# Kernel optimization log

Measured on AMD Instinct MI355X. Metric: run time of the kernel, lower is better.

The kernel has to match this reference:

```python
import jax, jax.numpy as jnp
import numpy as np

B, TA, TB, DIN, DEMB = 32, 128, 1024, 1280, 512
LN_EPS = 1e-5
MM_EPS = 1e-6


def _param(key, shape, scale=0.02):
    return (jax.random.normal(key, shape, dtype=jnp.float32) * scale)


def setup_inputs() -> dict:
    key = jax.random.key(0)
    ks = jax.random.split(key, 24)
    inp = {
        'pep_esm': jax.random.normal(ks[0], (B, TA, DIN), dtype=jnp.float32),
        'rec_esm': jax.random.normal(ks[1], (B, TB, DIN), dtype=jnp.float32),
        'pep_mask': jax.random.randint(ks[2], (B, TA), 0, 2, dtype=jnp.int32),
        'rec_mask': jax.random.randint(ks[3], (B, TB), 0, 2, dtype=jnp.int32),
        'temperature': jnp.asarray(1.0, dtype=jnp.float32),
    }
    i = 4
    for pre in ('pep', 'rec'):
        inp[pre + '_pw'] = _param(ks[i], (DIN, DEMB)); i += 1
        inp[pre + '_pb'] = jnp.zeros((DEMB,), jnp.float32)
        inp[pre + '_f1w'] = _param(ks[i], (DEMB, DEMB)); i += 1
        inp[pre + '_f1b'] = jnp.zeros((DEMB,), jnp.float32)
        inp[pre + '_lng'] = jnp.ones((DEMB,), jnp.float32)
        inp[pre + '_lnb'] = jnp.zeros((DEMB,), jnp.float32)
        inp[pre + '_f2w'] = _param(ks[i], (DEMB, DEMB)); i += 1
        inp[pre + '_f2b'] = jnp.zeros((DEMB,), jnp.float32)
    return inp


def _encode(x, pw, pb, f1w, f1b, lng, lnb, f2w, f2b):
    # projection -> (Linear, ReLU, LayerNorm) -> final Linear (dropout=0 at eval)
    e = x @ pw + pb                                   # [b, t, DEMB]
    h = jax.nn.relu(e @ f1w + f1b)
    mu = h.mean(-1, keepdims=True)
    var = ((h - mu) ** 2).mean(-1, keepdims=True)
    h = (h - mu) * jax.lax.rsqrt(var + LN_EPS) * lng + lnb
    out = h @ f2w + f2b
    return out / jnp.linalg.norm(out, axis=-1, keepdims=True)


def _masked_mean(t, mask, axis=-1):
    numer = jnp.where(mask, t, 0.0).sum(axis=axis)
    denom = jnp.maximum(mask.sum(axis=axis).astype(t.dtype), MM_EPS)
    return numer / denom


def reference(pep_esm, rec_esm, pep_mask, rec_mask, temperature,
              pep_pw, pep_pb, pep_f1w, pep_f1b, pep_lng, pep_lnb, pep_f2w, pep_f2b,
              rec_pw, rec_pb, rec_f1w, rec_f1b, rec_lng, rec_lnb, rec_f2w, rec_f2b):
    hA = _encode(pep_esm, pep_pw, pep_pb, pep_f1w, pep_f1b, pep_lng, pep_lnb, pep_f2w, pep_f2b)
    hB = _encode(rec_esm, rec_pw, rec_pb, rec_f1w, rec_f1b, rec_lng, rec_lnb, rec_f2w, rec_f2b)
    mA = pep_mask.astype(bool)                        # [bA, tA]
    mB = rec_mask.astype(bool)                        # [bB, tB]
    # pairwise token similarity: [bA, bB, tA, tB]
    sim = jnp.einsum('atd,bsd->abts', hA, hB) / temperature
    cmask = mA[:, None, :, None] & mB[None, :, None, :]
    neg = jnp.finfo(sim.dtype).min
    sim_m = jnp.where(cmask, sim, neg)
    sA = sim_m.max(axis=-1)                            # [bA, bB, tA]
    sB = sim_m.max(axis=-2)                            # [bA, bB, tB]
    sim_scores_A = _masked_mean(sA, mA[:, None, :])    # [bA, bB]
    sim_scores_B = _masked_mean(sB, mB[None, :, :])    # [bA, bB]
    return sim_scores_A, sim_scores_B
```

## Files before the change

### kernel.cpp

```cpp
#include <hip/hip_runtime.h>
#include <float.h>
#include <stddef.h>
#include <stdint.h>

#define DIN_   1280
#define DEMB_  512
#define NBAT_  32
#define TA_    128
#define TB_    1024
#define LN_EPS_ 1e-5f

using short8  = __attribute__((ext_vector_type(8))) short;
using ushort8 = __attribute__((ext_vector_type(8))) unsigned short;
using f32x4   = __attribute__((ext_vector_type(4))) float;

typedef const __attribute__((address_space(1))) unsigned int gu32;
typedef __attribute__((address_space(3))) unsigned int lu32;

__device__ __forceinline__ void gld_lds16(const void* g, void* l) {
    __builtin_amdgcn_global_load_lds((gu32*)g, (lu32*)l, 16, 0, 0);
}

__device__ __forceinline__ unsigned short f2bf(float x) {
    unsigned u = __float_as_uint(x);
    u += 0x7FFFu + ((u >> 16) & 1u);
    return (unsigned short)(u >> 16);
}
__device__ __forceinline__ float bf2f(unsigned short u) {
    return __uint_as_float((unsigned)u << 16);
}
__device__ __forceinline__ int clampi(int v, int hi) {
    return v < 0 ? 0 : (v > hi ? hi : v);
}

__global__ __launch_bounds__(64) void compact_idx_kernel(
    const int* __restrict__ mask, int T, int* __restrict__ idx, int* __restrict__ cnt)
{
    const int b = blockIdx.x, lane = threadIdx.x;
    const int base = b * T;
    int run = 0;
    for (int c = 0; c < T; c += 64) {
        int m = mask[base + c + lane] != 0;
        unsigned long long bal = __ballot(m);
        int pos = run + __popcll(bal & ((1ull << lane) - 1ull));
        idx[base + c + lane] = m ? pos : -1;
        run += __popcll(bal);
    }
    if (lane == 0) cnt[b] = run;
}

__global__ __launch_bounds__(64) void offsets_kernel(
    const int* __restrict__ cntA, const int* __restrict__ cntB,
    int* __restrict__ offA, int* __restrict__ offB, int* __restrict__ tot)
{
    if (threadIdx.x == 0) {
        int s = 0;
        for (int i = 0; i < NBAT_; ++i) { offA[i] = s; s += cntA[i]; }
        tot[0] = s;
        s = 0;
        for (int i = 0; i < NBAT_; ++i) { offB[i] = s; s += cntB[i]; }
        tot[1] = s;
    }
}

__global__ __launch_bounds__(256) void srcrows_kernel(
    const int* __restrict__ idx, const int* __restrict__ off, int shift,
    int* __restrict__ srcrows)
{
    int r = blockIdx.x * 256 + threadIdx.x;
    int d = idx[r];
    if (d >= 0) srcrows[off[r >> shift] + d] = r;
}

struct WPack { const float* src[4]; unsigned short* dst[4]; };
__global__ __launch_bounds__(256) void wtrans_multi_kernel(WPack p, int K, int N)
{
    __shared__ float tile[32][33];
    const float* W = p.src[blockIdx.z];
    unsigned short* Wt = p.dst[blockIdx.z];
    const int k0 = blockIdx.x * 32, n0 = blockIdx.y * 32;
    const int r = threadIdx.x >> 5, c = threadIdx.x & 31;
    #pragma unroll
    for (int i = 0; i < 4; ++i)
        tile[r + i * 8][c] = W[(size_t)(k0 + r + i * 8) * N + n0 + c];
    __syncthreads();
    #pragma unroll
    for (int i = 0; i < 4; ++i)
        Wt[(size_t)(n0 + r + i * 8) * K + k0 + c] = f2bf(tile[c][r + i * 8]);
}

struct EncDual {
    const unsigned short* A[2];
    const unsigned short* Wt[2];
    const float* bias[2];
    unsigned short* C[2];
    const int* Nr[2];
};
struct ProjDual {
    const float* A[2];
    const unsigned short* Wt[2];
    const float* bias[2];
    unsigned short* C[2];
    const int* srcrows[2];
    const int* Nr[2];
    int Mmax[2];
};
struct LnDual { unsigned short* h[2]; const float* g[2]; const float* b[2]; const int* Nr[2]; };
struct L2Dual { const unsigned short* h[2]; unsigned short* o[2]; const int* Nr[2]; };

template<int K, bool RELU>
__global__ __launch_bounds__(512, 4) void egemm_bf16_dual(EncDual P)
{
    const int side = blockIdx.y;
    const int bid = blockIdx.x;
    const int row0 = (bid >> 2) * 128, col0 = (bid & 3) * 128;
    if (row0 >= *P.Nr[side]) return;
    const unsigned short* A = P.A[side];
    const unsigned short* Wt = P.Wt[side];
    const float* bias = P.bias[side];
    unsigned short* C = P.C[side];

    __shared__ __align__(16) unsigned char Abuf[128 * 64 * 2];
    __shared__ __align__(16) unsigned char Bbuf[128 * 64 * 2];
    const int t = threadIdx.x;
    const int wave = t >> 6, lane = t & 63;
    const int wr = wave >> 2, wc = wave & 3;
    const int cl = lane & 15, rg = lane >> 4;

    const int pr0 = t >> 3, pq0 = t & 7;
    const int pr1 = pr0 + 64;
    const int ks0 = ((pq0 ^ (pr0 & 7)) * 8);
    const int ks1 = ((pq0 ^ (pr1 & 7)) * 8);
    const unsigned short* Aglob = A + (size_t)row0 * K;
    const unsigned short* Bglob = Wt + (size_t)col0 * K;

    int aoff[4], asw[4], boff[2], bsw[2];
    #pragma unroll
    for (int m = 0; m < 4; ++m) {
        int r = wr * 64 + m * 16 + cl;
        aoff[m] = r * 128; asw[m] = (r & 7) << 4;
    }
    #pragma unroll
    for (int n = 0; n < 2; ++n) {
        int c = wc * 32 + n * 16 + cl;
        boff[n] = c * 128; bsw[n] = (c & 7) << 4;
    }

    f32x4 acc[4][2];
    #pragma unroll
    for (int m = 0; m < 4; ++m) {
        acc[m][0] = (f32x4){0.f, 0.f, 0.f, 0.f};
        acc[m][1] = (f32x4){0.f, 0.f, 0.f, 0.f};
    }
    for (int k0 = 0; k0 < K; k0 += 64) {
        gld_lds16(Aglob + (size_t)pr0 * K + k0 + ks0, Abuf + t * 16);
        gld_lds16(Aglob + (size_t)pr1 * K + k0 + ks1, Abuf + (t + 512) * 16);
        gld_lds16(Bglob + (size_t)pr0 * K + k0 + ks0, Bbuf + t * 16);
        gld_lds16(Bglob + (size_t)pr1 * K + k0 + ks1, Bbuf + (t + 512) * 16);
        __syncthreads();
        #pragma unroll
        for (int h = 0; h < 2; ++h) {
            const int cb = h * 64 + rg * 16;
            short8 av[4], bv[2];
            #pragma unroll
            for (int m = 0; m < 4; ++m)
                av[m] = *(const short8*)(Abuf + aoff[m] + (cb ^ asw[m]));
            #pragma unroll
            for (int n = 0; n < 2; ++n)
                bv[n] = *(const short8*)(Bbuf + boff[n] + (cb ^ bsw[n]));
            #pragma unroll
            for (int m = 0; m < 4; ++m)
                #pragma unroll
                for (int n = 0; n < 2; ++n)
                    acc[m][n] = __builtin_amdgcn_mfma_f32_16x16x32_bf16(
                        av[m], bv[n], acc[m][n], 0, 0, 0);
        }
        __syncthreads();
    }
    const float b0 = bias[col0 + wc * 32 + cl];
    const float b1 = bias[col0 + wc * 32 + 16 + cl];
    #pragma unroll
    for (int m = 0; m < 4; ++m)
        #pragma unroll
        for (int j = 0; j < 4; ++j) {
            int row = row0 + wr * 64 + m * 16 + rg * 4 + j;
            float v0 = acc[m][0][j] + b0;
            float v1 = acc[m][1][j] + b1;
            if (RELU) { v0 = fmaxf(v0, 0.f); v1 = fmaxf(v1, 0.f); }
            C[(size_t)row * DEMB_ + col0 + wc * 32 + cl]      = f2bf(v0);
            C[(size_t)row * DEMB_ + col0 + wc * 32 + 16 + cl] = f2bf(v1);
        }
}

template<int K, bool RELU>
__global__ __launch_bounds__(512, 4) void egemm_f32a_g_dual(ProjDual P)
{
    const int side = blockIdx.y;
    const int bid = blockIdx.x;
    const int row0 = (bid >> 2) * 128, col0 = (bid & 3) * 128;
    if (row0 >= *P.Nr[side]) return;
    const float* A = P.A[side];
    const unsigned short* Wt = P.Wt[side];
    const float* bias = P.bias[side];
    unsigned short* C = P.C[side];
    const int* srcrows = P.srcrows[side];
    const int Mmax = P.Mmax[side];

    __shared__ __align__(16) unsigned char Abuf[128 * 64 * 2];
    __shared__ __align__(16) unsigned char Bbuf[128 * 64 * 2];
    const int t = threadIdx.x;
    const int wave = t >> 6, lane = t & 63;
    const int wr = wave >> 2, wc = wave & 3;
    const int cl = lane & 15, rg = lane >> 4;

    const int pr0 = t >> 3, pq0 = t & 7;
    const int pr1 = pr0 + 64;
    const int ks0 = ((pq0 ^ (pr0 & 7)) * 8);
    const int ks1 = ((pq0 ^ (pr1 & 7)) * 8);
    const int ad0 = pr0 * 128 + ((pq0 ^ (pr0 & 7)) << 4);
    const int ad1 = pr1 * 128 + ((pq0 ^ (pr1 & 7)) << 4);
    const int sr0 = clampi(srcrows[row0 + pr0], Mmax - 1);
    const int sr1 = clampi(srcrows[row0 + pr1], Mmax - 1);
    const float* Ar0 = A + (size_t)sr0 * K;
    const float* Ar1 = A + (size_t)sr1 * K;
    const unsigned short* Bglob = Wt + (size_t)col0 * K;

    int aoff[4], asw[4], boff[2], bsw[2];
    #pragma unroll
    for (int m = 0; m < 4; ++m) {
        int r = wr * 64 + m * 16 + cl;
        aoff[m] = r * 128; asw[m] = (r & 7) << 4;
    }
    #pragma unroll
    for (int n = 0; n < 2; ++n) {
        int c = wc * 32 + n * 16 + cl;
        boff[n] = c * 128; bsw[n] = (c & 7) << 4;
    }

    f32x4 acc[4][2];
    #pragma unroll
    for (int m = 0; m < 4; ++m) {
        acc[m][0] = (f32x4){0.f, 0.f, 0.f, 0.f};
        acc[m][1] = (f32x4){0.f, 0.f, 0.f, 0.f};
    }
    for (int k0 = 0; k0 < K; k0 += 64) {
        gld_lds16(Bglob + (size_t)pr0 * K + k0 + ks0, Bbuf + t * 16);
        gld_lds16(Bglob + (size_t)pr1 * K + k0 + ks1, Bbuf + (t + 512) * 16);
        {
            const float* s0 = Ar0 + k0 + pq0 * 8;
            const float* s1 = Ar1 + k0 + pq0 * 8;
            float4 u0 = *(const float4*)(s0), u1 = *(const float4*)(s0 + 4);
            float4 u2 = *(const float4*)(s1), u3 = *(const float4*)(s1 + 4);
            ushort8 w0, w1;
            w0[0] = f2bf(u0.x); w0[1] = f2bf(u0.y); w0[2] = f2bf(u0.z); w0[3] = f2bf(u0.w);
            w0[4] = f2bf(u1.x); w0[5] = f2bf(u1.y); w0[6] = f2bf(u1.z); w0[7] = f2bf(u1.w);
            w1[0] = f2bf(u2.x); w1[1] = f2bf(u2.y); w1[2] = f2bf(u2.z); w1[3] = f2bf(u2.w);
            w1[4] = f2bf(u3.x); w1[5] = f2bf(u3.y); w1[6] = f2bf(u3.z); w1[7] = f2bf(u3.w);
            *(ushort8*)(Abuf + ad0) = w0;
            *(ushort8*)(Abuf + ad1) = w1;
        }
        __syncthreads();
        #pragma unroll
        for (int h = 0; h < 2; ++h) {
            const int cb = h * 64 + rg * 16;
            short8 av[4], bv[2];
            #pragma unroll
            for (int m = 0; m < 4; ++m)
                av[m] = *(const short8*)(Abuf + aoff[m] + (cb ^ asw[m]));
            #pragma unroll
            for (int n = 0; n < 2; ++n)
                bv[n] = *(const short8*)(Bbuf + boff[n] + (cb ^ bsw[n]));
            #pragma unroll
            for (int m = 0; m < 4; ++m)
                #pragma unroll
                for (int n = 0; n < 2; ++n)
                    acc[m][n] = __builtin_amdgcn_mfma_f32_16x16x32_bf16(
                        av[m], bv[n], acc[m][n], 0, 0, 0);
        }
        __syncthreads();
    }
    const float b0 = bias[col0 + wc * 32 + cl];
    const float b1 = bias[col0 + wc * 32 + 16 + cl];
    #pragma unroll
    for (int m = 0; m < 4; ++m)
        #pragma unroll
        for (int j = 0; j < 4; ++j) {
            int row = row0 + wr * 64 + m * 16 + rg * 4 + j;
            float v0 = acc[m][0][j] + b0;
            float v1 = acc[m][1][j] + b1;
            if (RELU) { v0 = fmaxf(v0, 0.f); v1 = fmaxf(v1, 0.f); }
            C[(size_t)row * DEMB_ + col0 + wc * 32 + cl]      = f2bf(v0);
            C[(size_t)row * DEMB_ + col0 + wc * 32 + 16 + cl] = f2bf(v1);
        }
}

__global__ __launch_bounds__(256) void ln_bf16_dual(LnDual P)
{
    const int side = blockIdx.y;
    const int lane = threadIdx.x & 63;
    const int row = blockIdx.x * 4 + (threadIdx.x >> 6);
    if (row >= *P.Nr[side]) return;
    unsigned short* p = P.h[side] + (size_t)row * DEMB_;
    const float* g = P.g[side];
    const float* b = P.b[side];
    ushort8 v = *(const ushort8*)(p + lane * 8);
    float x[8];
    #pragma unroll
    for (int i = 0; i < 8; ++i) x[i] = bf2f(v[i]);
    float s = 0.f;
    #pragma unroll
    for (int i = 0; i < 8; ++i) s += x[i];
    #pragma unroll
    for (int d = 32; d >= 1; d >>= 1) s += __shfl_xor(s, d);
    float mu = s * (1.f / DEMB_);
    float sq = 0.f;
    #pragma unroll
    for (int i = 0; i < 8; ++i) { float dd = x[i] - mu; sq += dd * dd; }
    #pragma unroll
    for (int d = 32; d >= 1; d >>= 1) sq += __shfl_xor(sq, d);
    float rs = 1.f / sqrtf(sq * (1.f / DEMB_) + LN_EPS_);
    float4 g0 = *(const float4*)(g + lane * 8);
    float4 g1 = *(const float4*)(g + lane * 8 + 4);
    float4 b0 = *(const float4*)(b + lane * 8);
    float4 b1 = *(const float4*)(b + lane * 8 + 4);
    float gg[8] = {g0.x, g0.y, g0.z, g0.w, g1.x, g1.y, g1.z, g1.w};
    float bb[8] = {b0.x, b0.y, b0.z, b0.w, b1.x, b1.y, b1.z, b1.w};
    ushort8 o;
    #pragma unroll
    for (int i = 0; i < 8; ++i) o[i] = f2bf((x[i] - mu) * rs * gg[i] + bb[i]);
    *(ushort8*)(p + lane * 8) = o;
}

__global__ __launch_bounds__(256) void l2norm_bf16_dual(L2Dual P)
{
    const int side = blockIdx.y;
    const int lane = threadIdx.x & 63;
    const int row = blockIdx.x * 4 + (threadIdx.x >> 6);
    if (row >= *P.Nr[side]) return;
    const unsigned short* p = P.h[side] + (size_t)row * DEMB_;
    ushort8 v = *(const ushort8*)(p + lane * 8);
    float x[8];
    #pragma unroll
    for (int i = 0; i < 8; ++i) x[i] = bf2f(v[i]);
    float sq = 0.f;
    #pragma unroll
    for (int i = 0; i < 8; ++i) sq += x[i] * x[i];
    #pragma unroll
    for (int d = 32; d >= 1; d >>= 1) sq += __shfl_xor(sq, d);
    float rs = 1.f / sqrtf(sq);
    ushort8 w;
    #pragma unroll
    for (int i = 0; i < 8; ++i) w[i] = f2bf(x[i] * rs);
    *(ushort8*)(P.o[side] + (size_t)row * DEMB_ + lane * 8) = w;
}

__global__ __launch_bounds__(128, 3) void sim_part_kernel(
    const unsigned short* __restrict__ hA,
    const unsigned short* __restrict__ hB,
    const int* __restrict__ offA, const int* __restrict__ cntA,
    const int* __restrict__ offB, const int* __restrict__ cntB,
    const float* __restrict__ temp,
    float* __restrict__ rowmax_ws,
    float* __restrict__ colmax_ws)
{
    __shared__ __align__(16) unsigned char Abuf[64 * 64 * 2];
    __shared__ __align__(16) unsigned char Bbuf[128 * 64 * 2];
    __shared__ float rowpart[2][64];

    const int bid = blockIdx.x;
    const int g = (bid & 7) * 2048 + (bid >> 3);
    const int b = g >> 9;
    const int a = (g >> 4) & 31;
    const int at = (g >> 3) & 1, a0 = at << 6;
    const int s0t = g & 7, s0 = s0t << 7;

    const int nBb = cntB[b];
    if (s0 >= nBb) return;
    const int nAa = cntA[a];
    if (a0 >= nAa) return;

    const int t = threadIdx.x;
    const int w = t >> 6, lane = t & 63;
    const int cl = lane & 15, rg = lane >> 4;
    const float invT = 1.0f / temp[0];

    const int pr = t >> 3, pq = t & 7;
    const int ks = (pq ^ (pr & 7)) * 8;
    const int abase = offA[a] + a0 + pr;
    const int bbase = offB[b] + s0 + pr;
    const unsigned short* Ap[4];
    const unsigned short* Bp[8];
    #pragma unroll
    for (int i = 0; i < 4; ++i)
        Ap[i] = hA + (size_t)clampi(abase + 16 * i, NBAT_ * TA_ - 1) * DEMB_ + ks;
    #pragma unroll
    for (int i = 0; i < 8; ++i)
        Bp[i] = hB + (size_t)clampi(bbase + 16 * i, NBAT_ * TB_ - 1) * DEMB_ + ks;

    unsigned mabits = 0;
    #pragma unroll
    for (int m = 0; m < 4; ++m)
        #pragma unroll
        for (int j = 0; j < 4; ++j)
            if (a0 + m * 16 + rg * 4 + j < nAa) mabits |= 1u << (m * 4 + j);
    int mb[4];
    #pragma unroll
    for (int n = 0; n < 4; ++n)
        mb[n] = (s0 + w * 64 + n * 16 + cl) < nBb;

    int aoff[4], asw[4], boff[4], bsw[4];
    #pragma unroll
    for (int m = 0; m < 4; ++m) {
        int r = m * 16 + cl;
        aoff[m] = r * 128; asw[m] = (r & 7) << 4;
    }
    #pragma unroll
    for (int n = 0; n < 4; ++n) {
        int c = w * 64 + n * 16 + cl;
        boff[n] = c * 128; bsw[n] = (c & 7) << 4;
    }

    f32x4 acc[4][4];
    #pragma unroll
    for (int m = 0; m < 4; ++m)
        #pragma unroll
        for (int n = 0; n < 4; ++n)
            acc[m][n] = (f32x4){0.f, 0.f, 0.f, 0.f};

    for (int k0 = 0; k0 < DEMB_; k0 += 64) {
        #pragma unroll
        for (int i = 0; i < 4; ++i)
            gld_lds16(Ap[i] + k0, Abuf + (t + 128 * i) * 16);
        #pragma unroll
        for (int i = 0; i < 8; ++i)
            gld_lds16(Bp[i] + k0, Bbuf + (t + 128 * i) * 16);
        __syncthreads();
        #pragma unroll
        for (int h = 0; h < 2; ++h) {
            const int cb = h * 64 + rg * 16;
            short8 av[4], bv[4];
            #pragma unroll
            for (int m = 0; m < 4; ++m)
                av[m] = *(const short8*)(Abuf + aoff[m] + (cb ^ asw[m]));
            #pragma unroll
            for (int n = 0; n < 4; ++n)
                bv[n] = *(const short8*)(Bbuf + boff[n] + (cb ^ bsw[n]));
            #pragma unroll
            for (int m = 0; m < 4; ++m)
                #pragma unroll
                for (int n = 0; n < 4; ++n)
                    acc[m][n] = __builtin_amdgcn_mfma_f32_16x16x32_bf16(
                        av[m], bv[n], acc[m][n], 0, 0, 0);
        }
        __syncthreads();
    }
    float rmax[4][4];
    float cmax[4] = {-FLT_MAX, -FLT_MAX, -FLT_MAX, -FLT_MAX};
    #pragma unroll
    for (int m = 0; m < 4; ++m)
        #pragma unroll
        for (int j = 0; j < 4; ++j) {
            const bool ra = (mabits >> (m * 4 + j)) & 1;
            float rm = -FLT_MAX;
            #pragma unroll
            for (int n = 0; n < 4; ++n) {
                float v = (ra && mb[n]) ? acc[m][n][j] * invT : -FLT_MAX;
                rm = fmaxf(rm, v);
                cmax[n] = fmaxf(cmax[n], v);
            }
            rmax[m][j] = rm;
        }
    #pragma unroll
    for (int d = 1; d < 16; d <<= 1)
        #pragma unroll
        for (int m = 0; m < 4; ++m)
            #pragma unroll
            for (int j = 0; j < 4; ++j)
                rmax[m][j] = fmaxf(rmax[m][j], __shfl_xor(rmax[m][j], d));
    if (cl == 0) {
        #pragma unroll
        for (int m = 0; m < 4; ++m)
            #pragma unroll
            for (int j = 0; j < 4; ++j)
                rowpart[w][m * 16 + rg * 4 + j] = rmax[m][j];
    }
    #pragma unroll
    for (int n = 0; n < 4; ++n) {
        cmax[n] = fmaxf(cmax[n], __shfl_xor(cmax[n], 16));
        cmax[n] = fmaxf(cmax[n], __shfl_xor(cmax[n], 32));
    }
    if (rg == 0) {
        float* cw = colmax_ws + ((size_t)((a * NBAT_ + b) * 2 + at)) * TB_ + s0;
        #pragma unroll
        for (int n = 0; n < 4; ++n)
            cw[w * 64 + n * 16 + cl] = cmax[n];
    }
    __syncthreads();
    if (t < 64) {
        float r = fmaxf(rowpart[0][t], rowpart[1][t]);
        rowmax_ws[(((size_t)(a * NBAT_ + b)) * 8 + s0t) * 128 + a0 + t] = r;
    }
}

__global__ __launch_bounds__(256) void sim_reduce_kernel(
    const float* __restrict__ rowmax_ws, const float* __restrict__ colmax_ws,
    const int* __restrict__ cntA, const int* __restrict__ cntB,
    float* __restrict__ out)
{
    __shared__ float red[4][2];
    const int bid = blockIdx.x;
    const int a = bid >> 5, b = bid & 31;
    const int t = threadIdx.x, lane = t & 63, wave = t >> 6;
    const int nAa = cntA[a], nBb = cntB[b];
    const int nt = (nBb + 127) >> 7;

    float numA = 0.f, sumB = 0.f;
    if (t < 128 && t < nAa) {
        const float* rp = rowmax_ws + ((size_t)(a * NBAT_ + b)) * 8 * 128 + t;
        float r = -FLT_MAX;
        for (int s = 0; s < nt; ++s) r = fmaxf(r, rp[s * 128]);
        numA = r;
    }
    const float* cp0 = colmax_ws + ((size_t)(a * NBAT_ + b)) * 2 * TB_;
    const float* cp1 = cp0 + TB_;
    const bool two = nAa > 64;
    #pragma unroll
    for (int i = 0; i < 4; ++i) {
        int s = t + i * 256;
        if (s < nBb) {
            float v = cp0[s];
            if (two) v = fmaxf(v, cp1[s]);
            sumB += v;
        }
    }
    #pragma unroll
    for (int d = 32; d >= 1; d >>= 1) {
        numA += __shfl_xor(numA, d);
        sumB += __shfl_xor(sumB, d);
    }
    if (lane == 0) { red[wave][0] = numA; red[wave][1] = sumB; }
    __syncthreads();
    if (t == 0) {
        float n  = red[0][0] + red[1][0] + red[2][0] + red[3][0];
        float nb = red[0][1] + red[1][1] + red[2][1] + red[3][1];
        out[a * NBAT_ + b] = n / fmaxf((float)nAa, 1e-6f);
        out[NBAT_ * NBAT_ + a * NBAT_ + b] = nb / fmaxf((float)nBb, 1e-6f);
    }
}

extern "C" void kernel_launch(void* const* d_in, const int* in_sizes, int n_in,
                              void* d_out, int out_size, void* d_ws, size_t ws_size,
                              hipStream_t stream)
{
    const float* pep_esm  = (const float*)d_in[0];
    const float* rec_esm  = (const float*)d_in[1];
    const int*   pep_mask = (const int*)d_in[2];
    const int*   rec_mask = (const int*)d_in[3];
    const float* temp     = (const float*)d_in[4];
    const float* pep_pw  = (const float*)d_in[5];
    const float* pep_pb  = (const float*)d_in[6];
    const float* pep_f1w = (const float*)d_in[7];
    const float* pep_f1b = (const float*)d_in[8];
    const float* pep_lng = (const float*)d_in[9];
    const float* pep_lnb = (const float*)d_in[10];
    const float* pep_f2w = (const float*)d_in[11];
    const float* pep_f2b = (const float*)d_in[12];
    const float* rec_pw  = (const float*)d_in[13];
    const float* rec_pb  = (const float*)d_in[14];
    const float* rec_f1w = (const float*)d_in[15];
    const float* rec_f1b = (const float*)d_in[16];
    const float* rec_lng = (const float*)d_in[17];
    const float* rec_lnb = (const float*)d_in[18];
    const float* rec_f2w = (const float*)d_in[19];
    const float* rec_f2b = (const float*)d_in[20];
    float* out = (float*)d_out;

    const int Mr = NBAT_ * TB_;
    const int Mp = NBAT_ * TA_;

    char* base = (char*)d_ws;
    unsigned short* R1    = (unsigned short*)(base);
    unsigned short* R2    = (unsigned short*)(base + ((size_t)32 << 20));
    unsigned short* hB_c  = (unsigned short*)(base + ((size_t)64 << 20));
    unsigned short* hA_c  = (unsigned short*)(base + ((size_t)96 << 20));
    unsigned short* wts   = (unsigned short*)(base + ((size_t)101 << 20));
    unsigned short* rec_pwt  = wts;
    unsigned short* pep_pwt  = rec_pwt + 512 * 1280;
    unsigned short* rec_f1wt = pep_pwt + 512 * 1280;
    unsigned short* rec_f2wt = rec_f1wt + 512 * 512;
    unsigned short* pep_f1wt = rec_f2wt + 512 * 512;
    unsigned short* pep_f2wt = pep_f1wt + 512 * 512;
    unsigned short* P1 = (unsigned short*)(base + ((size_t)106 << 20));
    unsigned short* P2 = (unsigned short*)(base + ((size_t)110 << 20));
    float* rowmax_ws = (float*)(base + ((size_t)106 << 20));
    float* colmax_ws = (float*)(base + ((size_t)110 << 20));
    int* idxA = (int*)(base + ((size_t)118 << 20));
    int* idxB = idxA + Mp;
    int* cntA = idxB + Mr;
    int* cntB = cntA + NBAT_;
    int* offA = cntB + NBAT_;
    int* offB = offA + NBAT_;
    int* tot  = offB + NBAT_;
    int* srcA = tot + 2;
    int* srcB = srcA + Mp;

    dim3 b256(256);
    compact_idx_kernel<<<dim3(NBAT_), dim3(64), 0, stream>>>(pep_mask, TA_, idxA, cntA);
    compact_idx_kernel<<<dim3(NBAT_), dim3(64), 0, stream>>>(rec_mask, TB_, idxB, cntB);
    offsets_kernel<<<dim3(1), dim3(64), 0, stream>>>(cntA, cntB, offA, offB, tot);
    srcrows_kernel<<<dim3(Mp / 256), b256, 0, stream>>>(idxA, offA, 7, srcA);
    srcrows_kernel<<<dim3(Mr / 256), b256, 0, stream>>>(idxB, offB, 10, srcB);

    {
        WPack p1; p1.src[0] = rec_pw; p1.dst[0] = rec_pwt;
                  p1.src[1] = pep_pw; p1.dst[1] = pep_pwt;
                  p1.src[2] = rec_pw; p1.dst[2] = rec_pwt;
                  p1.src[3] = rec_pw; p1.dst[3] = rec_pwt;
        wtrans_multi_kernel<<<dim3(DIN_ / 32, DEMB_ / 32, 2), b256, 0, stream>>>(p1, DIN_, DEMB_);
        WPack p2; p2.src[0] = rec_f1w; p2.dst[0] = rec_f1wt;
                  p2.src[1] = rec_f2w; p2.dst[1] = rec_f2wt;
                  p2.src[2] = pep_f1w; p2.dst[2] = pep_f1wt;
                  p2.src[3] = pep_f2w; p2.dst[3] = pep_f2wt;
        wtrans_multi_kernel<<<dim3(DEMB_ / 32, DEMB_ / 32, 4), b256, 0, stream>>>(p2, DEMB_, DEMB_);
    }

    const int* NrRec = tot + 1;
    const int* NrPep = tot;
    const dim3 ggrid((Mr / 128) * 4, 2);
    const dim3 ngrid(Mr / 4, 2);

    {
        ProjDual P;
        P.A[0] = rec_esm;  P.A[1] = pep_esm;
        P.Wt[0] = rec_pwt; P.Wt[1] = pep_pwt;
        P.bias[0] = rec_pb; P.bias[1] = pep_pb;
        P.C[0] = R1; P.C[1] = P1;
        P.srcrows[0] = srcB; P.srcrows[1] = srcA;
        P.Nr[0] = NrRec; P.Nr[1] = NrPep;
        P.Mmax[0] = Mr; P.Mmax[1] = Mp;
        egemm_f32a_g_dual<DIN_, false><<<ggrid, dim3(512), 0, stream>>>(P);
    }
    {
        EncDual P;
        P.A[0] = R1; P.A[1] = P1;
        P.Wt[0] = rec_f1wt; P.Wt[1] = pep_f1wt;
        P.bias[0] = rec_f1b; P.bias[1] = pep_f1b;
        P.C[0] = R2; P.C[1] = P2;
        P.Nr[0] = NrRec; P.Nr[1] = NrPep;
        egemm_bf16_dual<DEMB_, true><<<ggrid, dim3(512), 0, stream>>>(P);
    }
    {
        LnDual P;
        P.h[0] = R2; P.h[1] = P2;
        P.g[0] = rec_lng; P.g[1] = pep_lng;
        P.b[0] = rec_lnb; P.b[1] = pep_lnb;
        P.Nr[0] = NrRec; P.Nr[1] = NrPep;
        ln_bf16_dual<<<ngrid, b256, 0, stream>>>(P);
    }
    {
        EncDual P;
        P.A[0] = R2; P.A[1] = P2;
        P.Wt[0] = rec_f2wt; P.Wt[1] = pep_f2wt;
        P.bias[0] = rec_f2b; P.bias[1] = pep_f2b;
        P.C[0] = R1; P.C[1] = P1;
        P.Nr[0] = NrRec; P.Nr[1] = NrPep;
        egemm_bf16_dual<DEMB_, false><<<ggrid, dim3(512), 0, stream>>>(P);
    }
    {
        L2Dual P;
        P.h[0] = R1; P.h[1] = P1;
        P.o[0] = hB_c; P.o[1] = hA_c;
        P.Nr[0] = NrRec; P.Nr[1] = NrPep;
        l2norm_bf16_dual<<<ngrid, b256, 0, stream>>>(P);
    }

    sim_part_kernel<<<dim3(NBAT_ * NBAT_ * 2 * 8), dim3(128), 0, stream>>>(
        hA_c, hB_c, offA, cntA, offB, cntB, temp, rowmax_ws, colmax_ws);
    sim_reduce_kernel<<<dim3(NBAT_ * NBAT_), b256, 0, stream>>>(
        rowmax_ws, colmax_ws, cntA, cntB, out);
}
```

Measured before the change: 264.4 us.

## Double-buffer LDS tiles in similarity GEMM to overlap loads with MFMA

New measurement: 302.0 us. 1.14x slower.

```diff
diff --git a/kernel.cpp b/kernel.cpp
--- a/kernel.cpp
+++ b/kernel.cpp
@@ -363,8 +363,8 @@
     float* __restrict__ rowmax_ws,
     float* __restrict__ colmax_ws)
 {
-    __shared__ __align__(16) unsigned char Abuf[64 * 64 * 2];
-    __shared__ __align__(16) unsigned char Bbuf[128 * 64 * 2];
+    __shared__ __align__(16) unsigned char Abuf[2 * 64 * 64 * 2];
+    __shared__ __align__(16) unsigned char Bbuf[2 * 128 * 64 * 2];
     __shared__ float rowpart[2][64];
 
     const int bid = blockIdx.x;
@@ -427,24 +427,42 @@
         for (int n = 0; n < 4; ++n)
             acc[m][n] = (f32x4){0.f, 0.f, 0.f, 0.f};
 
-    for (int k0 = 0; k0 < DEMB_; k0 += 64) {
-        #pragma unroll
-        for (int i = 0; i < 4; ++i)
-            gld_lds16(Ap[i] + k0, Abuf + (t + 128 * i) * 16);
-        #pragma unroll
-        for (int i = 0; i < 8; ++i)
-            gld_lds16(Bp[i] + k0, Bbuf + (t + 128 * i) * 16);
-        __syncthreads();
+    #pragma unroll
+    for (int i = 0; i < 4; ++i)
+        gld_lds16(Ap[i], Abuf + (t + 128 * i) * 16);
+    #pragma unroll
+    for (int i = 0; i < 8; ++i)
+        gld_lds16(Bp[i], Bbuf + (t + 128 * i) * 16);
+
+    int cur = 0;
+    for (int k = 0; k < 8; ++k) {
+        if (k < 7) {
+            const int k1 = (k + 1) * 64;
+            const int poA = (cur ^ 1) * 8192;
+            const int poB = (cur ^ 1) * 16384;
+            #pragma unroll
+            for (int i = 0; i < 4; ++i)
+                gld_lds16(Ap[i] + k1, Abuf + poA + (t + 128 * i) * 16);
+            #pragma unroll
+            for (int i = 0; i < 8; ++i)
+                gld_lds16(Bp[i] + k1, Bbuf + poB + (t + 128 * i) * 16);
+            asm volatile("s_waitcnt vmcnt(12)" ::: "memory");
+        } else {
+            asm volatile("s_waitcnt vmcnt(0)" ::: "memory");
+        }
+        __builtin_amdgcn_s_barrier();
+        const int boA = cur * 8192;
+        const int boB = cur * 16384;
         #pragma unroll
         for (int h = 0; h < 2; ++h) {
             const int cb = h * 64 + rg * 16;
             short8 av[4], bv[4];
             #pragma unroll
             for (int m = 0; m < 4; ++m)
-                av[m] = *(const short8*)(Abuf + aoff[m] + (cb ^ asw[m]));
+                av[m] = *(const short8*)(Abuf + boA + aoff[m] + (cb ^ asw[m]));
             #pragma unroll
             for (int n = 0; n < 4; ++n)
-                bv[n] = *(const short8*)(Bbuf + boff[n] + (cb ^ bsw[n]));
+                bv[n] = *(const short8*)(Bbuf + boB + boff[n] + (cb ^ bsw[n]));
             #pragma unroll
             for (int m = 0; m < 4; ++m)
                 #pragma unroll
@@ -452,7 +470,9 @@
                     acc[m][n] = __builtin_amdgcn_mfma_f32_16x16x32_bf16(
                         av[m], bv[n], acc[m][n], 0, 0, 0);
         }
-        __syncthreads();
+        asm volatile("s_waitcnt lgkmcnt(0)" ::: "memory");
+        __builtin_amdgcn_s_barrier();
+        cur ^= 1;
     }
     float rmax[4][4];
     float cmax[4] = {-FLT_MAX, -FLT_MAX, -FLT_MAX, -FLT_MAX};
```

## Use a single wave per 64x128 sim tile with 4x8 MFMA accumulators

Applied to the files above, without the earlier changes.

Measured after the change: 272.4 us. 3.0% more time.

```diff
diff --git a/kernel.cpp b/kernel.cpp
--- a/kernel.cpp
+++ b/kernel.cpp
@@ -354,7 +354,7 @@
     *(ushort8*)(P.o[side] + (size_t)row * DEMB_ + lane * 8) = w;
 }
 
-__global__ __launch_bounds__(128, 3) void sim_part_kernel(
+__global__ __launch_bounds__(64, 2) void sim_part_kernel(
     const unsigned short* __restrict__ hA,
     const unsigned short* __restrict__ hB,
     const int* __restrict__ offA, const int* __restrict__ cntA,
@@ -365,7 +365,6 @@
 {
     __shared__ __align__(16) unsigned char Abuf[64 * 64 * 2];
     __shared__ __align__(16) unsigned char Bbuf[128 * 64 * 2];
-    __shared__ float rowpart[2][64];
 
     const int bid = blockIdx.x;
     const int g = (bid & 7) * 2048 + (bid >> 3);
@@ -380,22 +379,21 @@
     if (a0 >= nAa) return;
 
     const int t = threadIdx.x;
-    const int w = t >> 6, lane = t & 63;
-    const int cl = lane & 15, rg = lane >> 4;
+    const int cl = t & 15, rg = t >> 4;
     const float invT = 1.0f / temp[0];
 
-    const int pr = t >> 3, pq = t & 7;
-    const int ks = (pq ^ (pr & 7)) * 8;
-    const int abase = offA[a] + a0 + pr;
-    const int bbase = offB[b] + s0 + pr;
-    const unsigned short* Ap[4];
-    const unsigned short* Bp[8];
-    #pragma unroll
-    for (int i = 0; i < 4; ++i)
-        Ap[i] = hA + (size_t)clampi(abase + 16 * i, NBAT_ * TA_ - 1) * DEMB_ + ks;
+    const int tr = t >> 3, tq = t & 7;
+    const int ks = (tq ^ tr) * 8;
+    const int abase = offA[a] + a0 + tr;
+    const int bbase = offB[b] + s0 + tr;
+    const unsigned short* Ap[8];
+    const unsigned short* Bp[16];
     #pragma unroll
     for (int i = 0; i < 8; ++i)
-        Bp[i] = hB + (size_t)clampi(bbase + 16 * i, NBAT_ * TB_ - 1) * DEMB_ + ks;
+        Ap[i] = hA + (size_t)clampi(abase + 8 * i, NBAT_ * TA_ - 1) * DEMB_ + ks;
+    #pragma unroll
+    for (int i = 0; i < 16; ++i)
+        Bp[i] = hB + (size_t)clampi(bbase + 8 * i, NBAT_ * TB_ - 1) * DEMB_ + ks;
 
     unsigned mabits = 0;
     #pragma unroll
@@ -403,59 +401,61 @@
         #pragma unroll
         for (int j = 0; j < 4; ++j)
             if (a0 + m * 16 + rg * 4 + j < nAa) mabits |= 1u << (m * 4 + j);
-    int mb[4];
-    #pragma unroll
-    for (int n = 0; n < 4; ++n)
-        mb[n] = (s0 + w * 64 + n * 16 + cl) < nBb;
-
-    int aoff[4], asw[4], boff[4], bsw[4];
+    int mb[8];
+    #pragma unroll
+    for (int n = 0; n < 8; ++n)
+        mb[n] = (s0 + n * 16 + cl) < nBb;
+
+    int aoff[4], asw[4], boff[8], bsw[8];
     #pragma unroll
     for (int m = 0; m < 4; ++m) {
         int r = m * 16 + cl;
         aoff[m] = r * 128; asw[m] = (r & 7) << 4;
     }
     #pragma unroll
-    for (int n = 0; n < 4; ++n) {
-        int c = w * 64 + n * 16 + cl;
+    for (int n = 0; n < 8; ++n) {
+        int c = n * 16 + cl;
         boff[n] = c * 128; bsw[n] = (c & 7) << 4;
     }
 
-    f32x4 acc[4][4];
+    f32x4 acc[4][8];
     #pragma unroll
     for (int m = 0; m < 4; ++m)
         #pragma unroll
-        for (int n = 0; n < 4; ++n)
+        for (int n = 0; n < 8; ++n)
             acc[m][n] = (f32x4){0.f, 0.f, 0.f, 0.f};
 
     for (int k0 = 0; k0 < DEMB_; k0 += 64) {
         #pragma unroll
-        for (int i = 0; i < 4; ++i)
-            gld_lds16(Ap[i] + k0, Abuf + (t + 128 * i) * 16);
-        #pragma unroll
         for (int i = 0; i < 8; ++i)
-            gld_lds16(Bp[i] + k0, Bbuf + (t + 128 * i) * 16);
+            gld_lds16(Ap[i] + k0, Abuf + (t + 64 * i) * 16);
+        #pragma unroll
+        for (int i = 0; i < 16; ++i)
+            gld_lds16(Bp[i] + k0, Bbuf + (t + 64 * i) * 16);
         __syncthreads();
         #pragma unroll
         for (int h = 0; h < 2; ++h) {
             const int cb = h * 64 + rg * 16;
-            short8 av[4], bv[4];
+            short8 av[4], bv[8];
             #pragma unroll
             for (int m = 0; m < 4; ++m)
                 av[m] = *(const short8*)(Abuf + aoff[m] + (cb ^ asw[m]));
             #pragma unroll
-            for (int n = 0; n < 4; ++n)
+            for (int n = 0; n < 8; ++n)
                 bv[n] = *(const short8*)(Bbuf + boff[n] + (cb ^ bsw[n]));
             #pragma unroll
             for (int m = 0; m < 4; ++m)
                 #pragma unroll
-                for (int n = 0; n < 4; ++n)
+                for (int n = 0; n < 8; ++n)
                     acc[m][n] = __builtin_amdgcn_mfma_f32_16x16x32_bf16(
                         av[m], bv[n], acc[m][n], 0, 0, 0);
         }
         __syncthreads();
     }
     float rmax[4][4];
-    float cmax[4] = {-FLT_MAX, -FLT_MAX, -FLT_MAX, -FLT_MAX};
+    float cmax[8];
+    #pragma unroll
+    for (int n = 0; n < 8; ++n) cmax[n] = -FLT_MAX;
     #pragma unroll
     for (int m = 0; m < 4; ++m)
         #pragma unroll
@@ -463,7 +463,7 @@
             const bool ra = (mabits >> (m * 4 + j)) & 1;
             float rm = -FLT_MAX;
             #pragma unroll
-            for (int n = 0; n < 4; ++n) {
+            for (int n = 0; n < 8; ++n) {
                 float v = (ra && mb[n]) ? acc[m][n][j] * invT : -FLT_MAX;
                 rm = fmaxf(rm, v);
                 cmax[n] = fmaxf(cmax[n], v);
@@ -478,27 +478,23 @@
             for (int j = 0; j < 4; ++j)
                 rmax[m][j] = fmaxf(rmax[m][j], __shfl_xor(rmax[m][j], d));
     if (cl == 0) {
+        float* rw = rowmax_ws + (((size_t)(a * NBAT_ + b)) * 8 + s0t) * 128 + a0;
         #pragma unroll
         for (int m = 0; m < 4; ++m)
             #pragma unroll
             for (int j = 0; j < 4; ++j)
-                rowpart[w][m * 16 + rg * 4 + j] = rmax[m][j];
-    }
-    #pragma unroll
-    for (int n = 0; n < 4; ++n) {
+                rw[m * 16 + rg * 4 + j] = rmax[m][j];
+    }
+    #pragma unroll
+    for (int n = 0; n < 8; ++n) {
         cmax[n] = fmaxf(cmax[n], __shfl_xor(cmax[n], 16));
         cmax[n] = fmaxf(cmax[n], __shfl_xor(cmax[n], 32));
     }
     if (rg == 0) {
         float* cw = colmax_ws + ((size_t)((a * NBAT_ + b) * 2 + at)) * TB_ + s0;
         #pragma unroll
-        for (int n = 0; n < 4; ++n)
-            cw[w * 64 + n * 16 + cl] = cmax[n];
-    }
-    __syncthreads();
-    if (t < 64) {
-        float r = fmaxf(rowpart[0][t], rowpart[1][t]);
-        rowmax_ws[(((size_t)(a * NBAT_ + b)) * 8 + s0t) * 128 + a0 + t] = r;
+        for (int n = 0; n < 8; ++n)
+            cw[n * 16 + cl] = cmax[n];
     }
 }
 
@@ -674,7 +670,7 @@
         l2norm_bf16_dual<<<ngrid, b256, 0, stream>>>(P);
     }
 
-    sim_part_kernel<<<dim3(NBAT_ * NBAT_ * 2 * 8), dim3(128), 0, stream>>>(
+    sim_part_kernel<<<dim3(NBAT_ * NBAT_ * 2 * 8), dim3(64), 0, stream>>>(
         hA_c, hB_c, offA, cntA, offB, cntB, temp, rowmax_ws, colmax_ws);
     sim_reduce_kernel<<<dim3(NBAT_ * NBAT_), b256, 0, stream>>>(
         rowmax_ws, colmax_ws, cntA, cntB, out);
```
